# Optimization experiments

Measured on AMD Instinct MI355X. Metric: run time of the kernel, lower is better.

## Reference

```python
import jax, jax.numpy as jnp
import numpy as np

NUM_CHARS = 128
BATCH = 8192
SEQ = 40
HIDDEN = 256


def setup_inputs() -> dict:
    key = jax.random.key(0)
    k1, k2, k3, k4 = jax.random.split(key, 4)
    inputs = jax.random.randint(k1, (BATCH, SEQ), 0, NUM_CHARS, dtype=jnp.int32)
    s_in = 1.0 / np.sqrt(NUM_CHARS)
    s_h = 1.0 / np.sqrt(HIDDEN)
    Wx = jax.random.normal(k2, (NUM_CHARS, 4 * HIDDEN), dtype=jnp.float32) * s_in
    Wh = jax.random.normal(k3, (HIDDEN, 4 * HIDDEN), dtype=jnp.float32) * s_h
    # keras unit_forget_bias: forget-gate bias initialized to 1
    b = jnp.concatenate([
        jnp.zeros((HIDDEN,), jnp.float32),
        jnp.ones((HIDDEN,), jnp.float32),
        jnp.zeros((2 * HIDDEN,), jnp.float32),
    ])
    Wd = jax.random.normal(k4, (HIDDEN, NUM_CHARS), dtype=jnp.float32) * s_h
    bd = jnp.zeros((NUM_CHARS,), jnp.float32)
    return {"inputs": inputs, "Wx": Wx, "Wh": Wh, "b": b, "Wd": Wd, "bd": bd}


def reference(inputs, Wx, Wh, b, Wd, bd):
    # one-hot encode: [B, T, V]
    x = jax.nn.one_hot(inputs, Wx.shape[0], dtype=jnp.float32)
    B = x.shape[0]
    H = Wh.shape[0]

    def step(carry, xt):
        h, c = carry
        z = xt @ Wx + h @ Wh + b  # [B, 4H], keras gate order i,f,g,o
        i, f, g, o = jnp.split(z, 4, axis=-1)
        c = jax.nn.sigmoid(f) * c + jax.nn.sigmoid(i) * jnp.tanh(g)
        h = jax.nn.sigmoid(o) * jnp.tanh(c)
        return (h, c), None

    h0 = jnp.zeros((B, H), jnp.float32)
    c0 = jnp.zeros((B, H), jnp.float32)
    (h, _), _ = jax.lax.scan(step, (h0, c0), jnp.swapaxes(x, 0, 1))  # scan over T
    logits = h @ Wd + bd  # [B, V]
    return jax.nn.softmax(logits, axis=-1)
```

## Files before the change

kernel.cpp:

```cpp
#include <hip/hip_runtime.h>
#include <stdint.h>

#define NUM_CHARS 128
#define BATCH 8192
#define SEQ 40
#define HIDDEN 256
#define ZDIM 1024
#define SH 264

typedef __bf16 bf16x8 __attribute__((ext_vector_type(8)));
typedef float floatx16 __attribute__((ext_vector_type(16)));

__device__ __forceinline__ unsigned short f2bf(float f) {
    union { float f; uint32_t u; } v; v.f = f;
    uint32_t u = v.u;
    u += 0x7FFFu + ((u >> 16) & 1u);
    return (unsigned short)(u >> 16);
}

__device__ __forceinline__ void gl_lds16(const unsigned short* g, unsigned short* l) {
    __builtin_amdgcn_global_load_lds(
        (const __attribute__((address_space(1))) unsigned int*)g,
        (__attribute__((address_space(3))) unsigned int*)l, 16, 0, 0);
}

__global__ void prep_wh(const float* __restrict__ Wh, unsigned short* __restrict__ out) {
    int idx = blockIdx.x * blockDim.x + threadIdx.x;
    int j = idx & 7;
    int lane = (idx >> 3) & 63;
    int kk = (idx >> 9) & 15;
    int ntile = idx >> 13;
    int k = kk * 16 + ((lane >> 5) << 3) + j;
    int n = (ntile << 5) + (lane & 31);
    out[idx] = f2bf(Wh[k * ZDIM + n]);
}

__global__ void prep_wxb4(const float* __restrict__ Wx, const float* __restrict__ b,
                          unsigned short* __restrict__ out) {
    int idx = blockIdx.x * blockDim.x + threadIdx.x;
    int v = idx >> 10;
    int n = (idx >> 2) & 255;
    int g = idx & 3;
    out[idx] = f2bf(Wx[v * ZDIM + g * 256 + n] + b[g * 256 + n]);
}

__global__ void prep_wd(const float* __restrict__ Wd, unsigned short* __restrict__ out) {
    int idx = blockIdx.x * blockDim.x + threadIdx.x;
    int j = idx & 7;
    int lane = (idx >> 3) & 63;
    int kk = (idx >> 9) & 15;
    int nt = idx >> 13;
    int k = kk * 16 + ((lane >> 5) << 3) + j;
    int n = (nt << 5) + (lane & 31);
    out[idx] = f2bf(Wd[k * NUM_CHARS + n]);
}

#define ROWI(i) (((i) & 3) + 8 * ((i) >> 2) + rbase)

__device__ __forceinline__ void gates_store(floatx16 (&acc)[4], floatx16& c_st,
                                            unsigned short* hb, int rbase, int hcol) {
    const float L2E = 1.4426950408889634f;
#pragma unroll
    for (int i = 0; i < 16; ++i) {
        float zi = acc[0][i], zf = acc[1][i], zg = acc[2][i], zo = acc[3][i];
        float si = __builtin_amdgcn_rcpf(1.f + __builtin_amdgcn_exp2f(-zi * L2E));
        float sf = __builtin_amdgcn_rcpf(1.f + __builtin_amdgcn_exp2f(-zf * L2E));
        float so = __builtin_amdgcn_rcpf(1.f + __builtin_amdgcn_exp2f(-zo * L2E));
        float tg = 1.f - 2.f * __builtin_amdgcn_rcpf(1.f + __builtin_amdgcn_exp2f(2.f * L2E * zg));
        float c = sf * c_st[i] + si * tg;
        c_st[i] = c;
        float tc = 1.f - 2.f * __builtin_amdgcn_rcpf(1.f + __builtin_amdgcn_exp2f(2.f * L2E * c));
        hb[ROWI(i) * SH + hcol] = f2bf(so * tc);
    }
}

#define MFMA4(AF, B0, B1, B2, B3)                                                   \
    acc[0] = __builtin_amdgcn_mfma_f32_32x32x16_bf16(AF, B0, acc[0], 0, 0, 0);      \
    acc[1] = __builtin_amdgcn_mfma_f32_32x32x16_bf16(AF, B1, acc[1], 0, 0, 0);      \
    acc[2] = __builtin_amdgcn_mfma_f32_32x32x16_bf16(AF, B2, acc[2], 0, 0, 0);      \
    acc[3] = __builtin_amdgcn_mfma_f32_32x32x16_bf16(AF, B3, acc[3], 0, 0, 0);

#define L_MFMA(KK) {                                                                 \
    bf16x8 af = *(const bf16x8*)&hbuf[abase + (KK) * 16];                            \
    bf16x8 b0 = *(const bf16x8*)&wlds[((((0 * 8 + w) << 2) + (KK)) << 9) + (lane << 3)]; \
    bf16x8 b1 = *(const bf16x8*)&wlds[((((1 * 8 + w) << 2) + (KK)) << 9) + (lane << 3)]; \
    bf16x8 b2 = *(const bf16x8*)&wlds[((((2 * 8 + w) << 2) + (KK)) << 9) + (lane << 3)]; \
    bf16x8 b3 = *(const bf16x8*)&wlds[((((3 * 8 + w) << 2) + (KK)) << 9) + (lane << 3)]; \
    MFMA4(af, b0, b1, b2, b3)                                                        \
}

#define R_MFMA(KK) {                                                                 \
    bf16x8 af = *(const bf16x8*)&hbuf[abase + (KK) * 16];                            \
    MFMA4(af, wr[0][(KK) - 4], wr[1][(KK) - 4], wr[2][(KK) - 4], wr[3][(KK) - 4])    \
}

#define S_MFMA(J) {                                                                  \
    bf16x8 af = *(const bf16x8*)&hbuf[abase + (J) * 16];                             \
    MFMA4(af, sw[((J) - 9) & 1][0], sw[((J) - 9) & 1][1],                            \
              sw[((J) - 9) & 1][2], sw[((J) - 9) & 1][3])                            \
    if ((J) + 2 <= 15) {                                                             \
        sw[((J) - 9) & 1][0] = *(const bf16x8*)(wsb[0] + (((J) + 2) << 9));          \
        sw[((J) - 9) & 1][1] = *(const bf16x8*)(wsb[1] + (((J) + 2) << 9));          \
        sw[((J) - 9) & 1][2] = *(const bf16x8*)(wsb[2] + (((J) + 2) << 9));          \
        sw[((J) - 9) & 1][3] = *(const bf16x8*)(wsb[3] + (((J) + 2) << 9));          \
    }                                                                                \
}

__global__ __launch_bounds__(512) void lstm_main(
    const int* __restrict__ inputs, const unsigned short* __restrict__ WhFrag,
    const unsigned short* __restrict__ WxbG, const unsigned short* __restrict__ WdFrag,
    const float* __restrict__ bd, float* __restrict__ out)
{
    __shared__ unsigned short wlds[32 * 4 * 512];
    __shared__ unsigned short hbuf[32 * SH];
    __shared__ int tok[32 * SEQ];
    __shared__ float red[2][4][32];

    const int tid = threadIdx.x;
    const int w = tid >> 6;
    const int lane = tid & 63;
    const int r0 = blockIdx.x * 32;

    for (int i = tid; i < 32 * SEQ; i += 512) tok[i] = inputs[r0 * SEQ + i];
#pragma unroll
    for (int k = 0; k < 16; ++k) {
        int f = w + (k << 3);
        gl_lds16(WhFrag + (((((f >> 2) << 4) + (f & 3)) << 9) + (lane << 3)),
                 &wlds[f << 9]);
    }

    const unsigned short* wsb[4];
#pragma unroll
    for (int g = 0; g < 4; ++g)
        wsb[g] = WhFrag + (((g * 8 + w) * 16) << 9) + (lane << 3);

    bf16x8 wr[4][5];
#pragma unroll
    for (int g = 0; g < 4; ++g)
#pragma unroll
        for (int rk = 0; rk < 5; ++rk)
            wr[g][rk] = *(const bf16x8*)(wsb[g] + ((4 + rk) << 9));

    const int hcol = (w << 5) + (lane & 31);
    const int rbase = 4 * (lane >> 5);
    const int abase = (lane & 31) * SH + ((lane >> 5) << 3);

    floatx16 c_st;
#pragma unroll
    for (int i = 0; i < 16; ++i) c_st[i] = 0.f;

    __syncthreads();

    uint2 xb[16];

    {
#pragma unroll
        for (int i = 0; i < 16; ++i)
            xb[i] = *(const uint2*)&WxbG[(tok[ROWI(i) * SEQ] << 10) + (hcol << 2)];
        floatx16 acc[4];
#pragma unroll
        for (int i = 0; i < 16; ++i) {
            uint32_t x = xb[i].x, y = xb[i].y;
            acc[0][i] = __uint_as_float(x << 16);
            acc[1][i] = __uint_as_float(x & 0xFFFF0000u);
            acc[2][i] = __uint_as_float(y << 16);
            acc[3][i] = __uint_as_float(y & 0xFFFF0000u);
        }
#pragma unroll
        for (int i = 0; i < 16; ++i)
            xb[i] = *(const uint2*)&WxbG[(tok[ROWI(i) * SEQ + 1] << 10) + (hcol << 2)];
        gates_store(acc, c_st, hbuf, rbase, hcol);
    }
    __syncthreads();

#pragma unroll 1
    for (int t = 1; t < SEQ; ++t) {
        floatx16 acc[4];
#pragma unroll
        for (int i = 0; i < 16; ++i) {
            uint32_t x = xb[i].x, y = xb[i].y;
            acc[0][i] = __uint_as_float(x << 16);
            acc[1][i] = __uint_as_float(x & 0xFFFF0000u);
            acc[2][i] = __uint_as_float(y << 16);
            acc[3][i] = __uint_as_float(y & 0xFFFF0000u);
        }
        __builtin_amdgcn_sched_barrier(0);

        bf16x8 sw[2][4];
#pragma unroll
        for (int s = 0; s < 2; ++s) {
            sw[s][0] = *(const bf16x8*)(wsb[0] + ((9 + s) << 9));
            sw[s][1] = *(const bf16x8*)(wsb[1] + ((9 + s) << 9));
            sw[s][2] = *(const bf16x8*)(wsb[2] + ((9 + s) << 9));
            sw[s][3] = *(const bf16x8*)(wsb[3] + ((9 + s) << 9));
        }

        L_MFMA(0) L_MFMA(1) L_MFMA(2) L_MFMA(3)
        R_MFMA(4) R_MFMA(5) R_MFMA(6) R_MFMA(7) R_MFMA(8)
        S_MFMA(9) S_MFMA(10) S_MFMA(11) S_MFMA(12)
        S_MFMA(13) S_MFMA(14) S_MFMA(15)

        __syncthreads();

        int tn = (t + 1 < SEQ) ? t + 1 : SEQ - 1;
#pragma unroll
        for (int i = 0; i < 16; ++i)
            xb[i] = *(const uint2*)&WxbG[(tok[ROWI(i) * SEQ + tn] << 10) + (hcol << 2)];

        gates_store(acc, c_st, hbuf, rbase, hcol);
        __syncthreads();
    }

    float* scratch = (float*)wlds;
    const int vt = w & 3;
    floatx16 accd;
    float p[16];
    float mx[16];
    {
#pragma unroll
        for (int i = 0; i < 16; ++i) accd[i] = 0.f;
        if (w < 4) {
            float bdv = bd[(vt << 5) + (lane & 31)];
#pragma unroll
            for (int i = 0; i < 16; ++i) accd[i] = bdv;
        }
        int kk0 = (w < 4) ? 0 : 8;
#pragma unroll
        for (int kk = 0; kk < 8; ++kk) {
            bf16x8 af = *(const bf16x8*)&hbuf[abase + (kk0 + kk) * 16];
            bf16x8 bfd = *(const bf16x8*)(WdFrag + ((((vt << 4) + kk0 + kk) << 6) + lane) * 8);
            accd = __builtin_amdgcn_mfma_f32_32x32x16_bf16(af, bfd, accd, 0, 0, 0);
        }
        if (w >= 4) {
#pragma unroll
            for (int i = 0; i < 16; ++i)
                scratch[((vt << 5) + ROWI(i)) * 32 + (lane & 31)] = accd[i];
        }
    }
    __syncthreads();
    if (w < 4) {
#pragma unroll
        for (int i = 0; i < 16; ++i)
            accd[i] += scratch[((vt << 5) + ROWI(i)) * 32 + (lane & 31)];
#pragma unroll
        for (int i = 0; i < 16; ++i) {
            float m = accd[i];
#pragma unroll
            for (int off = 1; off < 32; off <<= 1) m = fmaxf(m, __shfl_xor(m, off, 32));
            mx[i] = m;
        }
        if ((lane & 31) == 0) {
#pragma unroll
            for (int i = 0; i < 16; ++i) red[0][vt][ROWI(i)] = mx[i];
        }
    }
    __syncthreads();
    const float L2E = 1.4426950408889634f;
    if (w < 4) {
#pragma unroll
        for (int i = 0; i < 16; ++i) {
            int r = ROWI(i);
            float M = fmaxf(fmaxf(red[0][0][r], red[0][1][r]),
                            fmaxf(red[0][2][r], red[0][3][r]));
            float e = __builtin_amdgcn_exp2f((accd[i] - M) * L2E);
            p[i] = e;
            float s = e;
#pragma unroll
            for (int off = 1; off < 32; off <<= 1) s += __shfl_xor(s, off, 32);
            mx[i] = s;
        }
        if ((lane & 31) == 0) {
#pragma unroll
            for (int i = 0; i < 16; ++i) red[1][vt][ROWI(i)] = mx[i];
        }
    }
    __syncthreads();
    if (w < 4) {
#pragma unroll
        for (int i = 0; i < 16; ++i) {
            int r = ROWI(i);
            float tot = red[1][0][r] + red[1][1][r] + red[1][2][r] + red[1][3][r];
            out[(size_t)(r0 + r) * NUM_CHARS + (vt << 5) + (lane & 31)] =
                p[i] * __builtin_amdgcn_rcpf(tot);
        }
    }
}

extern "C" void kernel_launch(void* const* d_in, const int* in_sizes, int n_in,
                              void* d_out, int out_size, void* d_ws, size_t ws_size,
                              hipStream_t stream) {
    const int*   inputs = (const int*)d_in[0];
    const float* Wx = (const float*)d_in[1];
    const float* Wh = (const float*)d_in[2];
    const float* b  = (const float*)d_in[3];
    const float* Wd = (const float*)d_in[4];
    const float* bd = (const float*)d_in[5];
    float* out = (float*)d_out;

    unsigned short* WhFrag = (unsigned short*)d_ws;
    unsigned short* WxbG   = (unsigned short*)((char*)d_ws + (512 << 10));
    unsigned short* WdFrag = (unsigned short*)((char*)d_ws + (768 << 10));

    prep_wh  <<<262144 / 256, 256, 0, stream>>>(Wh, WhFrag);
    prep_wxb4<<<131072 / 256, 256, 0, stream>>>(Wx, b, WxbG);
    prep_wd  <<< 32768 / 256, 256, 0, stream>>>(Wd, WdFrag);
    lstm_main<<<256, 512, 0, stream>>>(inputs, WhFrag, WxbG, WdFrag, bd, out);
}
```

Before: 318.2 us.

## Double-buffer hidden state in LDS to drop one barrier per step

The hidden state buffer becomes two ping-pong buffers, so gates write the next h into the alternate buffer and the mid-step __syncthreads between the MFMA reads and the gate writes is removed. To fit the extra LDS, the LDS-resident Wh slice shrinks from 4 to 3 k-chunks per tile, and one more k-chunk per gate moves into registers (wr grows from 5 to 6 entries). The intent is to cut barrier stalls in the serial recurrence. The cost is higher register pressure, which may reduce occupancy or cause spills.

```diff
diff --git a/kernel.cpp b/kernel.cpp
--- a/kernel.cpp
+++ b/kernel.cpp
@@ -58,7 +58,7 @@
 #define ROWI(i) (((i) & 3) + 8 * ((i) >> 2) + rbase)
 
 __device__ __forceinline__ void gates_store(floatx16 (&acc)[4], floatx16& c_st,
-                                            unsigned short* hb, int rbase, int hcol) {
+                                            unsigned short* hn, int rbase, int hcol) {
     const float L2E = 1.4426950408889634f;
 #pragma unroll
     for (int i = 0; i < 16; ++i) {
@@ -70,7 +70,7 @@
         float c = sf * c_st[i] + si * tg;
         c_st[i] = c;
         float tc = 1.f - 2.f * __builtin_amdgcn_rcpf(1.f + __builtin_amdgcn_exp2f(2.f * L2E * c));
-        hb[ROWI(i) * SH + hcol] = f2bf(so * tc);
+        hn[ROWI(i) * SH + hcol] = f2bf(so * tc);
     }
 }
 
@@ -81,21 +81,21 @@
     acc[3] = __builtin_amdgcn_mfma_f32_32x32x16_bf16(AF, B3, acc[3], 0, 0, 0);
 
 #define L_MFMA(KK) {                                                                 \
-    bf16x8 af = *(const bf16x8*)&hbuf[abase + (KK) * 16];                            \
-    bf16x8 b0 = *(const bf16x8*)&wlds[((((0 * 8 + w) << 2) + (KK)) << 9) + (lane << 3)]; \
-    bf16x8 b1 = *(const bf16x8*)&wlds[((((1 * 8 + w) << 2) + (KK)) << 9) + (lane << 3)]; \
-    bf16x8 b2 = *(const bf16x8*)&wlds[((((2 * 8 + w) << 2) + (KK)) << 9) + (lane << 3)]; \
-    bf16x8 b3 = *(const bf16x8*)&wlds[((((3 * 8 + w) << 2) + (KK)) << 9) + (lane << 3)]; \
+    bf16x8 af = *(const bf16x8*)&hb[abase + (KK) * 16];                              \
+    bf16x8 b0 = *(const bf16x8*)&wlds[(((0 * 8 + w) * 3 + (KK)) << 9) + (lane << 3)];\
+    bf16x8 b1 = *(const bf16x8*)&wlds[(((1 * 8 + w) * 3 + (KK)) << 9) + (lane << 3)];\
+    bf16x8 b2 = *(const bf16x8*)&wlds[(((2 * 8 + w) * 3 + (KK)) << 9) + (lane << 3)];\
+    bf16x8 b3 = *(const bf16x8*)&wlds[(((3 * 8 + w) * 3 + (KK)) << 9) + (lane << 3)];\
     MFMA4(af, b0, b1, b2, b3)                                                        \
 }
 
 #define R_MFMA(KK) {                                                                 \
-    bf16x8 af = *(const bf16x8*)&hbuf[abase + (KK) * 16];                            \
-    MFMA4(af, wr[0][(KK) - 4], wr[1][(KK) - 4], wr[2][(KK) - 4], wr[3][(KK) - 4])    \
+    bf16x8 af = *(const bf16x8*)&hb[abase + (KK) * 16];                              \
+    MFMA4(af, wr[0][(KK) - 3], wr[1][(KK) - 3], wr[2][(KK) - 3], wr[3][(KK) - 3])    \
 }
 
 #define S_MFMA(J) {                                                                  \
-    bf16x8 af = *(const bf16x8*)&hbuf[abase + (J) * 16];                             \
+    bf16x8 af = *(const bf16x8*)&hb[abase + (J) * 16];                               \
     MFMA4(af, sw[((J) - 9) & 1][0], sw[((J) - 9) & 1][1],                            \
               sw[((J) - 9) & 1][2], sw[((J) - 9) & 1][3])                            \
     if ((J) + 2 <= 15) {                                                             \
@@ -111,8 +111,8 @@
     const unsigned short* __restrict__ WxbG, const unsigned short* __restrict__ WdFrag,
     const float* __restrict__ bd, float* __restrict__ out)
 {
-    __shared__ unsigned short wlds[32 * 4 * 512];
-    __shared__ unsigned short hbuf[32 * SH];
+    __shared__ unsigned short wlds[32 * 3 * 512];
+    __shared__ unsigned short hbuf[2][32 * SH];
     __shared__ int tok[32 * SEQ];
     __shared__ float red[2][4][32];
 
@@ -123,9 +123,10 @@
 
     for (int i = tid; i < 32 * SEQ; i += 512) tok[i] = inputs[r0 * SEQ + i];
 #pragma unroll
-    for (int k = 0; k < 16; ++k) {
+    for (int k = 0; k < 12; ++k) {
         int f = w + (k << 3);
-        gl_lds16(WhFrag + (((((f >> 2) << 4) + (f & 3)) << 9) + (lane << 3)),
+        int ntile = f / 3, kkL = f % 3;
+        gl_lds16(WhFrag + ((((ntile << 4) + kkL) << 9) + (lane << 3)),
                  &wlds[f << 9]);
     }
 
@@ -134,12 +135,12 @@
     for (int g = 0; g < 4; ++g)
         wsb[g] = WhFrag + (((g * 8 + w) * 16) << 9) + (lane << 3);
 
-    bf16x8 wr[4][5];
+    bf16x8 wr[4][6];
 #pragma unroll
     for (int g = 0; g < 4; ++g)
 #pragma unroll
-        for (int rk = 0; rk < 5; ++rk)
-            wr[g][rk] = *(const bf16x8*)(wsb[g] + ((4 + rk) << 9));
+        for (int rk = 0; rk < 6; ++rk)
+            wr[g][rk] = *(const bf16x8*)(wsb[g] + ((3 + rk) << 9));
 
     const int hcol = (w << 5) + (lane & 31);
     const int rbase = 4 * (lane >> 5);
@@ -169,12 +170,16 @@
 #pragma unroll
         for (int i = 0; i < 16; ++i)
             xb[i] = *(const uint2*)&WxbG[(tok[ROWI(i) * SEQ + 1] << 10) + (hcol << 2)];
-        gates_store(acc, c_st, hbuf, rbase, hcol);
-    }
-    __syncthreads();
-
+        gates_store(acc, c_st, hbuf[0], rbase, hcol);
+    }
+    __syncthreads();
+
+    int cur = 0;
 #pragma unroll 1
     for (int t = 1; t < SEQ; ++t) {
+        const unsigned short* hb = hbuf[cur];
+        unsigned short* hn = hbuf[cur ^ 1];
+
         floatx16 acc[4];
 #pragma unroll
         for (int i = 0; i < 16; ++i) {
@@ -195,23 +200,23 @@
             sw[s][3] = *(const bf16x8*)(wsb[3] + ((9 + s) << 9));
         }
 
-        L_MFMA(0) L_MFMA(1) L_MFMA(2) L_MFMA(3)
-        R_MFMA(4) R_MFMA(5) R_MFMA(6) R_MFMA(7) R_MFMA(8)
-        S_MFMA(9) S_MFMA(10) S_MFMA(11) S_MFMA(12)
-        S_MFMA(13) S_MFMA(14) S_MFMA(15)
-
-        __syncthreads();
+        L_MFMA(0) L_MFMA(1) L_MFMA(2)
+        R_MFMA(3) R_MFMA(4) R_MFMA(5) R_MFMA(6) R_MFMA(7) R_MFMA(8)
+        S_MFMA(9) S_MFMA(10) S_MFMA(11) S_MFMA(12) S_MFMA(13) S_MFMA(14) S_MFMA(15)
 
         int tn = (t + 1 < SEQ) ? t + 1 : SEQ - 1;
 #pragma unroll
         for (int i = 0; i < 16; ++i)
             xb[i] = *(const uint2*)&WxbG[(tok[ROWI(i) * SEQ + tn] << 10) + (hcol << 2)];
 
-        gates_store(acc, c_st, hbuf, rbase, hcol);
+        gates_store(acc, c_st, hn, rbase, hcol);
+
         __syncthreads();
+        cur ^= 1;
     }
 
     float* scratch = (float*)wlds;
+    const unsigned short* hb = hbuf[cur];
     const int vt = w & 3;
     floatx16 accd;
     float p[16];
@@ -227,7 +232,7 @@
         int kk0 = (w < 4) ? 0 : 8;
 #pragma unroll
         for (int kk = 0; kk < 8; ++kk) {
-            bf16x8 af = *(const bf16x8*)&hbuf[abase + (kk0 + kk) * 16];
+            bf16x8 af = *(const bf16x8*)&hb[abase + (kk0 + kk) * 16];
             bf16x8 bfd = *(const bf16x8*)(WdFrag + ((((vt << 4) + kk0 + kk) << 6) + lane) * 8);
             accd = __builtin_amdgcn_mfma_f32_32x32x16_bf16(af, bfd, accd, 0, 0, 0);
         }
```

New measurement: 322.8 us. No clear change (+1.5%).
